# Kernel tuning notes

Measured on AMD Instinct MI355X. Metric: run time of the kernel, lower is better.

The kernel has to match this reference:

```python
import jax, jax.numpy as jnp
import numpy as np

B, IMGS, PH, PW = 4, 4, 16, 16      # 4 groups, 4 images/group, 16x16 patches per image
P, C = 16, 3
N = IMGS * PH * PW                   # 1024 packed tokens per group
PATCH_DIM = C * P * P                # 768
DIM, HEADS, DHEAD, DEPTH = 768, 12, 64, 4
INNER = HEADS * DHEAD
MLP = 3072
POSMAX = 32                          # image_size // patch_size
NCLS = 1000
SCALE = DHEAD ** 0.5


def _ln(x, g):
    # torch LayerNorm with learned gamma, beta frozen at 0
    mu = jnp.mean(x, -1, keepdims=True)
    var = jnp.var(x, -1, keepdims=True)
    return (x - mu) * jax.lax.rsqrt(var + 1e-5) * g


def _qk_rmsnorm(t, g):
    # F.normalize(t, dim=-1) * sqrt(dhead) * gamma[h, 1, d]; t: (b,h,n,d), g: (h,d)
    nrm = jnp.sqrt(jnp.sum(t * t, -1, keepdims=True))
    return t / jnp.maximum(nrm, 1e-12) * SCALE * g[None, :, None, :]


def _attention(x, context, ln_g, Wq, Wkv, qg, kg, Wo, attn_mask):
    xn = _ln(x, ln_g)
    kv_in = xn if context is None else context  # context is NOT normed (matches torch)
    q = xn @ Wq
    k, v = jnp.split(kv_in @ Wkv, 2, axis=-1)
    split = lambda t: t.reshape(t.shape[0], t.shape[1], HEADS, DHEAD).transpose(0, 2, 1, 3)
    q, k, v = split(q), split(k), split(v)
    q = _qk_rmsnorm(q, qg)
    k = _qk_rmsnorm(k, kg)
    dots = jnp.einsum('bhid,bhjd->bhij', q, k)  # no 1/sqrt(d): scale lives in RMSNorm
    dots = jnp.where(attn_mask, dots, -jnp.finfo(dots.dtype).max)
    attn = jax.nn.softmax(dots, axis=-1)
    out = jnp.einsum('bhij,bhjd->bhid', attn, v)
    out = out.transpose(0, 2, 1, 3).reshape(x.shape[0], -1, INNER)
    return out @ Wo


def _forward(patches, emb_ln_g, W_emb, b_emb, emb_ln2_g, pos_h, pos_w,
             ln_attn_g, Wq, Wkv, qn_g, kn_g, Wo,
             ln_ff_g, W1, b1, W2, b2, final_ln_g,
             pool_q, pool_ln_g, pWq, pWkv, p_qn_g, p_kn_g, pWo,
             head_ln_g, W_head,
             patch_positions, image_ids, lengths):
    valid = jnp.arange(N)[None, :] < lengths[:, None]              # (B,N) True = real token
    same_img = image_ids[:, :, None] == image_ids[:, None, :]      # (B,i,j) block-diagonal
    attn_mask = (same_img & valid[:, None, :])[:, None]            # (B,1,i,j)

    x = _ln(patches, emb_ln_g) @ W_emb + b_emb
    x = _ln(x, emb_ln2_g)
    x = x + pos_h[patch_positions[..., 0]] + pos_w[patch_positions[..., 1]]

    for l in range(DEPTH):
        x = _attention(x, None, ln_attn_g[l], Wq[l], Wkv[l], qn_g[l], kn_g[l], Wo[l], attn_mask) + x
        h = jax.nn.gelu(_ln(x, ln_ff_g[l]) @ W1[l] + b1[l], approximate=False)
        x = h @ W2[l] + b2[l] + x
    x = _ln(x, final_ln_g)

    # attention pooling: one learned query per packed image
    queries = jnp.broadcast_to(pool_q, (x.shape[0], IMGS, DIM))
    pool_mask = ((jnp.arange(IMGS)[None, :, None] == image_ids[:, None, :]) & valid[:, None, :])[:, None]
    pooled = _attention(queries, x, pool_ln_g, pWq, pWkv, p_qn_g, p_kn_g, pWo, pool_mask) + queries
    return _ln(pooled, head_ln_g) @ W_head  # (B, IMGS, NCLS), mlp_head has no bias


def setup_inputs():
    key = jax.random.key(0)
    ks = jax.random.split(key, 20)
    rn = lambda k, shape, s=0.02: (jax.random.normal(k, shape) * s).astype(jnp.float32)

    patches = jax.random.normal(ks[0], (B, N, PATCH_DIM), dtype=jnp.float32)
    hh, ww = jnp.meshgrid(jnp.arange(PH), jnp.arange(PW), indexing='ij')
    pos = jnp.stack([hh.reshape(-1), ww.reshape(-1)], axis=-1)        # (256,2)
    patch_positions = jnp.broadcast_to(jnp.tile(pos, (IMGS, 1))[None], (B, N, 2)).astype(jnp.int32)
    image_ids = jnp.broadcast_to(jnp.repeat(jnp.arange(IMGS), PH * PW)[None], (B, N)).astype(jnp.int32)
    lengths = jnp.full((B,), N, dtype=jnp.int32)

    return dict(
        patches=patches, patch_positions=patch_positions, image_ids=image_ids, lengths=lengths,
        emb_ln_g=jnp.ones(PATCH_DIM, jnp.float32), W_emb=rn(ks[1], (PATCH_DIM, DIM)),
        b_emb=jnp.zeros(DIM, jnp.float32), emb_ln2_g=jnp.ones(DIM, jnp.float32),
        pos_h=rn(ks[2], (POSMAX, DIM), 1.0), pos_w=rn(ks[3], (POSMAX, DIM), 1.0),
        ln_attn_g=jnp.ones((DEPTH, DIM), jnp.float32),
        Wq=rn(ks[4], (DEPTH, DIM, INNER)), Wkv=rn(ks[5], (DEPTH, DIM, 2 * INNER)),
        qn_g=jnp.ones((DEPTH, HEADS, DHEAD), jnp.float32), kn_g=jnp.ones((DEPTH, HEADS, DHEAD), jnp.float32),
        Wo=rn(ks[6], (DEPTH, INNER, DIM)),
        ln_ff_g=jnp.ones((DEPTH, DIM), jnp.float32),
        W1=rn(ks[7], (DEPTH, DIM, MLP)), b1=jnp.zeros((DEPTH, MLP), jnp.float32),
        W2=rn(ks[8], (DEPTH, MLP, DIM)), b2=jnp.zeros((DEPTH, DIM), jnp.float32),
        final_ln_g=jnp.ones(DIM, jnp.float32),
        pool_q=rn(ks[9], (DIM,), 1.0), pool_ln_g=jnp.ones(DIM, jnp.float32),
        pWq=rn(ks[10], (DIM, INNER)), pWkv=rn(ks[11], (DIM, 2 * INNER)),
        p_qn_g=jnp.ones((HEADS, DHEAD), jnp.float32), p_kn_g=jnp.ones((HEADS, DHEAD), jnp.float32),
        pWo=rn(ks[12], (INNER, DIM)),
        head_ln_g=jnp.ones(DIM, jnp.float32), W_head=rn(ks[13], (DIM, NCLS)),
    )


def reference(patches, patch_positions, image_ids, lengths,
              emb_ln_g, W_emb, b_emb, emb_ln2_g, pos_h, pos_w,
              ln_attn_g, Wq, Wkv, qn_g, kn_g, Wo,
              ln_ff_g, W1, b1, W2, b2, final_ln_g,
              pool_q, pool_ln_g, pWq, pWkv, p_qn_g, p_kn_g, pWo,
              head_ln_g, W_head):
    return _forward(patches, emb_ln_g, W_emb, b_emb, emb_ln2_g, pos_h, pos_w,
                    ln_attn_g, Wq, Wkv, qn_g, kn_g, Wo,
                    ln_ff_g, W1, b1, W2, b2, final_ln_g,
                    pool_q, pool_ln_g, pWq, pWkv, p_qn_g, p_kn_g, pWo,
                    head_ln_g, W_head, patch_positions, image_ids, lengths)
```

## Files before the change

kernel.cpp:

```cpp
#include <hip/hip_runtime.h>
#include <hip/hip_bf16.h>
#include <math.h>

using bf16 = __hip_bfloat16;
typedef short s16x8 __attribute__((ext_vector_type(8)));
typedef short s16x4 __attribute__((ext_vector_type(4)));
typedef float f32x4 __attribute__((ext_vector_type(4)));

#define DEVI __device__ __forceinline__

static constexpr int NB    = 4;
static constexpr int NTOK  = 1024;
static constexpr int DIM   = 768;
static constexpr int NH    = 12;
static constexpr int MLPD  = 3072;
static constexpr int NLAYER= 4;
static constexpr int NIMG  = 4;
static constexpr int NCLS  = 1000;
static constexpr int MR    = NB * NTOK;
static constexpr size_t SLAB = (size_t)MR * 768;

DEVI float b2f(bf16 v){ return __bfloat162float(v); }
DEVI bf16  f2b(float v){ return __float2bfloat16(v); }
DEVI float bu2f(unsigned short u){ union{unsigned u32; float f;} w; w.u32 = ((unsigned)u)<<16; return w.f; }
DEVI unsigned short f2bu(float f){ bf16 b = f2b(f); return *(unsigned short*)&b; }

DEVI void async16(const void* g, void* l) {
  __builtin_amdgcn_global_load_lds((const __attribute__((address_space(1))) void*)g,
                                   (__attribute__((address_space(3))) void*)l, 16, 0, 0);
}

DEVI f32x4 mfma16(s16x8 a, s16x8 b, f32x4 c) {
  return __builtin_amdgcn_mfma_f32_16x16x32_bf16(a, b, c, 0, 0, 0);
}

template<int N> DEVI void waitcnt_vm() {
  if constexpr (N == 0)      asm volatile("s_waitcnt vmcnt(0)" ::: "memory");
  else if constexpr (N == 3) asm volatile("s_waitcnt vmcnt(3)" ::: "memory");
  else if constexpr (N == 4) asm volatile("s_waitcnt vmcnt(4)" ::: "memory");
  else if constexpr (N == 6) asm volatile("s_waitcnt vmcnt(6)" ::: "memory");
}

DEVI float block_sum(float v, float* scratch, int tid) {
  #pragma unroll
  for (int o = 32; o >= 1; o >>= 1) v += __shfl_xor(v, o);
  __syncthreads();
  if ((tid & 63) == 0) scratch[tid >> 6] = v;
  __syncthreads();
  return scratch[0] + scratch[1] + scratch[2] + scratch[3];
}

DEVI float block_max(float v, float* scratch, int tid) {
  #pragma unroll
  for (int o = 32; o >= 1; o >>= 1) v = fmaxf(v, __shfl_xor(v, o));
  __syncthreads();
  if ((tid & 63) == 0) scratch[tid >> 6] = v;
  __syncthreads();
  return fmaxf(fmaxf(scratch[0], scratch[1]), fmaxf(scratch[2], scratch[3]));
}

struct TEntry { const float* src; bf16* dst; int R, C, tiles, tC; };
struct TDesc  { TEntry e[22]; };

__global__ __launch_bounds__(256) void transpose_kernel(TDesc D, int nent) {
  int bid = blockIdx.x, ei = 0;
  while (ei < nent - 1 && bid >= D.e[ei].tiles) { bid -= D.e[ei].tiles; ++ei; }
  const TEntry E = D.e[ei];
  const int tr = bid / E.tC, tc = bid % E.tC;
  __shared__ unsigned short t[64][68];
  const int tid = threadIdx.x;
  {
    const int r = tid >> 4, c = (tid & 15) * 4;
    float4 v[4];
    #pragma unroll
    for (int p = 0; p < 4; ++p)
      v[p] = *(const float4*)(E.src + (size_t)(tr*64 + p*16 + r)*E.C + tc*64 + c);
    #pragma unroll
    for (int p = 0; p < 4; ++p) {
      unsigned short* dst = &t[p*16 + r][c];
      dst[0] = f2bu(v[p].x); dst[1] = f2bu(v[p].y); dst[2] = f2bu(v[p].z); dst[3] = f2bu(v[p].w);
    }
  }
  __syncthreads();
  #pragma unroll
  for (int p = 0; p < 2; ++p) {
    const int n = p*32 + (tid >> 3);
    const int r0 = (tid & 7) * 8;
    s16x8 o;
    #pragma unroll
    for (int i = 0; i < 8; ++i) o[i] = (short)t[r0 + i][n];
    *(s16x8*)((short*)E.dst + (size_t)(tc*64 + n)*E.R + tr*64 + r0) = o;
  }
}

__global__ __launch_bounds__(256) void ln768_kernel(const float* __restrict__ in,
    const float* __restrict__ g, bf16* __restrict__ out)
{
  __shared__ float scratch[4];
  const int row = blockIdx.x, tid = threadIdx.x;
  const float* p = in + (size_t)row*768;
  const float v0 = p[tid], v1 = p[tid+256], v2 = p[tid+512];
  const float s  = block_sum(v0+v1+v2, scratch, tid);
  const float ss = block_sum(v0*v0+v1*v1+v2*v2, scratch, tid);
  const float mu = s * (1.0f/768.0f);
  const float var = ss * (1.0f/768.0f) - mu*mu;
  const float rstd = rsqrtf(var + 1e-5f);
  bf16* o = out + (size_t)row*768;
  o[tid]     = f2b((v0-mu)*rstd*g[tid]);
  o[tid+256] = f2b((v1-mu)*rstd*g[tid+256]);
  o[tid+512] = f2b((v2-mu)*rstd*g[tid+512]);
}

template<int HAS_BIAS>
__global__ __launch_bounds__(256) void res2_ln_kernel(float* __restrict__ x,
    const float* __restrict__ P, const float* __restrict__ bias,
    const float* __restrict__ g, bf16* __restrict__ xn)
{
  __shared__ float scratch[4];
  const int row = blockIdx.x, tid = threadIdx.x;
  const size_t base = (size_t)row*768;
  const float* p0 = P + base;
  const float* p1 = P + SLAB + base;
  float* xr = x + base;
  float v[3];
  #pragma unroll
  for (int i = 0; i < 3; ++i) {
    const int c = tid + i*256;
    float t = xr[c] + p0[c] + p1[c];
    if constexpr (HAS_BIAS) t += bias[c];
    v[i] = t;
    xr[c] = t;
  }
  const float s  = block_sum(v[0]+v[1]+v[2], scratch, tid);
  const float ss = block_sum(v[0]*v[0]+v[1]*v[1]+v[2]*v[2], scratch, tid);
  const float mu = s * (1.0f/768.0f);
  const float rstd = rsqrtf(ss*(1.0f/768.0f) - mu*mu + 1e-5f);
  bf16* o = xn + base;
  #pragma unroll
  for (int i = 0; i < 3; ++i) {
    const int c = tid + i*256;
    o[c] = f2b((v[i]-mu)*rstd*g[c]);
  }
}

__global__ __launch_bounds__(256) void ln_pos2_kernel(const float* __restrict__ P,
    const float* __restrict__ bias, const float* __restrict__ g,
    const float* __restrict__ pos_h, const float* __restrict__ pos_w,
    const int* __restrict__ ppos, float* __restrict__ out,
    const float* __restrict__ g2, bf16* __restrict__ xn)
{
  __shared__ float scratch[4];
  const int row = blockIdx.x, tid = threadIdx.x;
  const size_t base = (size_t)row*768;
  const float* p0 = P + base;
  const float* p1 = P + SLAB + base;
  float v[3];
  #pragma unroll
  for (int i = 0; i < 3; ++i) {
    const int c = tid + i*256;
    v[i] = p0[c] + p1[c] + bias[c];
  }
  const float s  = block_sum(v[0]+v[1]+v[2], scratch, tid);
  const float ss = block_sum(v[0]*v[0]+v[1]*v[1]+v[2]*v[2], scratch, tid);
  const float mu = s * (1.0f/768.0f);
  const float rstd = rsqrtf(ss*(1.0f/768.0f) - mu*mu + 1e-5f);
  const int p0i = ppos[row*2], p1i = ppos[row*2+1];
  const float* ph = pos_h + (size_t)p0i*768;
  const float* pw = pos_w + (size_t)p1i*768;
  float* o = out + base;
  float xv[3];
  #pragma unroll
  for (int i = 0; i < 3; ++i) {
    const int c = tid + i*256;
    xv[i] = (v[i]-mu)*rstd*g[c] + ph[c] + pw[c];
    o[c] = xv[i];
  }
  const float s2  = block_sum(xv[0]+xv[1]+xv[2], scratch, tid);
  const float ss2 = block_sum(xv[0]*xv[0]+xv[1]*xv[1]+xv[2]*xv[2], scratch, tid);
  const float mu2 = s2 * (1.0f/768.0f);
  const float rstd2 = rsqrtf(ss2*(1.0f/768.0f) - mu2*mu2 + 1e-5f);
  bf16* on = xn + base;
  #pragma unroll
  for (int i = 0; i < 3; ++i) {
    const int c = tid + i*256;
    on[c] = f2b((xv[i]-mu2)*rstd2*g2[c]);
  }
}

template<int DO_BIAS, int DO_GELU, int OUT_BF16, int DO_RES, int NTILE, int SPLITK, int RMSQKV>
__global__ __launch_bounds__(256)
void gemm_mfma(const bf16* __restrict__ A, const bf16* __restrict__ BT,
               const float* __restrict__ bias, float* __restrict__ Cf,
               bf16* __restrict__ Cb,
               const float* __restrict__ qg, const float* __restrict__ kg,
               bf16* __restrict__ Qp, bf16* __restrict__ Kp, bf16* __restrict__ Vp,
               int M, int Nn, int K)
{
  constexpr int NF  = NTILE / 32;
  constexpr int PD  = 3;
  constexpr int LPI = 2 + NTILE/64;
  constexpr int VW  = (PD - 2) * LPI;
  __shared__ bf16 As[PD][64*64];
  __shared__ bf16 Bs[PD][(NTILE/2)*64];
  const int tid = threadIdx.x;
  const int wid = tid >> 6, lane = tid & 63;
  const int quad = lane >> 4, l15 = lane & 15;
  const int wy = wid >> 1, wx = wid & 1;

  const int gx  = gridDim.x;
  const int nwg = gx * gridDim.y;
  const int bid = blockIdx.y * gx + blockIdx.x;
  const int qq  = nwg >> 3, rm = nwg & 7;
  const int xcd = bid & 7,  li = bid >> 3;
  const int swz = (xcd < rm ? xcd * (qq + 1) : rm * (qq + 1) + (xcd - rm) * qq) + li;
  const int m0 = (swz / gx) * 128, n0 = (swz % gx) * NTILE;

  const int kz    = (SPLITK > 1) ? blockIdx.z : 0;
  const int kloc  = K / SPLITK;
  const int kbase = kz * kloc;

  const int rl = lane >> 3;
  const int cs = lane & 7;

  f32x4 acc[4][NF];
  #pragma unroll
  for (int i = 0; i < 4; ++i)
    #pragma unroll
    for (int j = 0; j < NF; ++j) acc[i][j] = (f32x4){0.f,0.f,0.f,0.f};

  auto stage = [&](int buf, int k0) {
    #pragma unroll
    for (int c = 0; c < 2; ++c) {
      const int rbase = wid*8 + c*32;
      const int r_abs = rbase + rl;
      const int ceff  = cs ^ (r_abs & 7);
      const int mg    = 2*r_abs + (ceff >> 2);
      const int jb    = (ceff & 3) * 16;
      async16((const char*)A + ((size_t)(m0 + mg)*K + k0)*2 + jb, (char*)As[buf] + rbase*128);
    }
    #pragma unroll
    for (int c = 0; c < NTILE/64; ++c) {
      const int rbase = wid*8 + c*32;
      const int r_abs = rbase + rl;
      const int ceff  = cs ^ (r_abs & 7);
      const int ng    = 2*r_abs + (ceff >> 2);
      const int jb    = (ceff & 3) * 16;
      async16((const char*)BT + ((size_t)(n0 + ng)*K + k0)*2 + jb, (char*)Bs[buf] + rbase*128);
    }
  };

  auto compute = [&](int cb) {
    s16x8 af[4], bfr[NF];
    #pragma unroll
    for (int mt = 0; mt < 4; ++mt) {
      const int m = wy*64 + mt*16 + l15;
      const int r = m >> 1;
      const int cq = (((m & 1) << 2) | quad) ^ (r & 7);
      af[mt] = *(const s16x8*)((const char*)As[cb] + r*128 + cq*16);
    }
    #pragma unroll
    for (int nt = 0; nt < NF; ++nt) {
      const int n = wx*(NTILE/2) + nt*16 + l15;
      const int r = n >> 1;
      const int cq = (((n & 1) << 2) | quad) ^ (r & 7);
      bfr[nt] = *(const s16x8*)((const char*)Bs[cb] + r*128 + cq*16);
    }
    #pragma unroll
    for (int mt = 0; mt < 4; ++mt)
      #pragma unroll
      for (int nt = 0; nt < NF; ++nt)
        acc[mt][nt] = mfma16(af[mt], bfr[nt], acc[mt][nt]);
  };

  const int nk = kloc >> 5;
  #pragma unroll
  for (int t = 0; t < PD - 1; ++t) stage(t, kbase + (t << 5));

  int cbuf = 0, sbuf = PD - 1;
  const int mainN = nk - (PD - 1);
  for (int kt = 0; kt < mainN; ++kt) {
    __builtin_amdgcn_sched_barrier(0);
    waitcnt_vm<VW>();
    __builtin_amdgcn_s_barrier();
    __builtin_amdgcn_sched_barrier(0);
    stage(sbuf, kbase + ((kt + PD - 1) << 5));
    compute(cbuf);
    cbuf = (cbuf + 1 == PD) ? 0 : cbuf + 1;
    sbuf = (sbuf + 1 == PD) ? 0 : sbuf + 1;
  }
  for (int kt = mainN; kt < nk; ++kt) {
    __builtin_amdgcn_sched_barrier(0);
    waitcnt_vm<0>();
    __builtin_amdgcn_s_barrier();
    __builtin_amdgcn_sched_barrier(0);
    compute(cbuf);
    cbuf = (cbuf + 1 == PD) ? 0 : cbuf + 1;
  }

  if constexpr (RMSQKV) {
    __shared__ float red[128][2];
    const int hg = n0 >> 6;
    const int region = hg / NH;
    const int h  = hg - region*NH;
    const int b  = m0 >> 10;
    const int bh = b*NH + h;
    const int tokb = m0 & (NTOK-1);
    if (region < 2) {
      float sl[4][4];
      #pragma unroll
      for (int mt = 0; mt < 4; ++mt)
        #pragma unroll
        for (int rr = 0; rr < 4; ++rr) {
          float ssq = 0.f;
          #pragma unroll
          for (int nt = 0; nt < NF; ++nt) ssq += acc[mt][nt][rr]*acc[mt][nt][rr];
          #pragma unroll
          for (int o = 1; o <= 8; o <<= 1) ssq += __shfl_xor(ssq, o);
          sl[mt][rr] = ssq;
        }
      if (l15 == 0) {
        #pragma unroll
        for (int mt = 0; mt < 4; ++mt)
          #pragma unroll
          for (int rr = 0; rr < 4; ++rr)
            red[wy*64 + mt*16 + quad*4 + rr][wx] = sl[mt][rr];
      }
      __syncthreads();
      const float* gp = (region == 0) ? (qg + n0) : (kg + (n0 - 768));
      bf16* outb = (region == 0) ? Qp : Kp;
      #pragma unroll
      for (int mt = 0; mt < 4; ++mt)
        #pragma unroll
        for (int rr = 0; rr < 4; ++rr) {
          const int rlc = wy*64 + mt*16 + quad*4 + rr;
          const float rn = 8.0f / fmaxf(sqrtf(red[rlc][0] + red[rlc][1]), 1e-12f);
          const int tok = tokb + rlc;
          #pragma unroll
          for (int nt = 0; nt < NF; ++nt) {
            const int d = wx*32 + nt*16 + l15;
            outb[((size_t)bh*NTOK + tok)*64 + d] = f2b(acc[mt][nt][rr]*rn*gp[d]);
          }
        }
    } else {
      #pragma unroll
      for (int mt = 0; mt < 4; ++mt)
        #pragma unroll
        for (int nt = 0; nt < NF; ++nt) {
          const int d = wx*32 + nt*16 + l15;
          const int tok = tokb + wy*64 + mt*16 + quad*4;
          s16x4 pk;
          #pragma unroll
          for (int rr = 0; rr < 4; ++rr) pk[rr] = (short)f2bu(acc[mt][nt][rr]);
          *(s16x4*)((short*)Vp + ((size_t)bh*64 + d)*NTOK + tok) = pk;
        }
    }
  } else {
    float* Cslab = (SPLITK > 1) ? (Cf + (size_t)kz * SLAB) : Cf;
    #pragma unroll
    for (int nt = 0; nt < NF; ++nt) {
      const int col = n0 + wx*(NTILE/2) + nt*16 + l15;
      float bv = 0.f;
      if constexpr (DO_BIAS) bv = bias[col];
      #pragma unroll
      for (int mt = 0; mt < 4; ++mt) {
        #pragma unroll
        for (int r = 0; r < 4; ++r) {
          const int row = m0 + wy*64 + mt*16 + quad*4 + r;
          float v = acc[mt][nt][r];
          if constexpr (DO_BIAS) v += bv;
          if constexpr (DO_GELU) v = 0.5f*v*(1.0f + erff(v*0.70710678118654752f));
          const size_t idx = (size_t)row*Nn + col;
          if constexpr (OUT_BF16) Cb[idx] = f2b(v);
          else if constexpr (DO_RES) Cslab[idx] += v;
          else Cslab[idx] = v;
        }
      }
    }
  }
}

template<int IN_BF16, int DO_BIAS>
__global__ __launch_bounds__(256) void smallm_gemm(const void* __restrict__ Xv,
    const float* __restrict__ W, const float* __restrict__ bias,
    float* __restrict__ out, int Nn)
{
  __shared__ float Xs[16*768];
  __shared__ float red[4][16][64];
  const int tid = threadIdx.x;
  if constexpr (IN_BF16) {
    const bf16* X = (const bf16*)Xv;
    for (int i = tid; i < 16*768; i += 256) Xs[i] = b2f(X[i]);
  } else {
    const float* X = (const float*)Xv;
    for (int i = tid; i < 16*768; i += 256) Xs[i] = X[i];
  }
  __syncthreads();
  const int cl = tid & 63, kg = tid >> 6;
  const int c = blockIdx.x*64 + cl;
  float acc[16];
  #pragma unroll
  for (int r = 0; r < 16; ++r) acc[r] = 0.f;
  if (c < Nn) {
    const int k0 = kg*192;
    #pragma unroll 4
    for (int k = k0; k < k0 + 192; ++k) {
      const float w = W[(size_t)k*Nn + c];
      #pragma unroll
      for (int r = 0; r < 16; ++r) acc[r] += Xs[r*768 + k] * w;
    }
  }
  #pragma unroll
  for (int r = 0; r < 16; ++r) red[kg][r][cl] = acc[r];
  __syncthreads();
  if (kg == 0 && c < Nn) {
    #pragma unroll
    for (int r = 0; r < 16; ++r) {
      float v = red[0][r][cl] + red[1][r][cl] + red[2][r][cl] + red[3][r][cl];
      if constexpr (DO_BIAS) v += bias[c];
      out[(size_t)r*Nn + c] = v;
    }
  }
}

__global__ __launch_bounds__(256) void attn_mfma(const bf16* __restrict__ Qb,
    const bf16* __restrict__ Kb, const bf16* __restrict__ VTb, bf16* __restrict__ Ob,
    const int* __restrict__ ids, const int* __restrict__ lens)
{
  __shared__ bf16 Ps[4][16*72];
  __shared__ int  ids_s[NTOK];
  const int qt = blockIdx.x, h = blockIdx.y, b = blockIdx.z;
  const int tid = threadIdx.x;
  const int wid = tid >> 6, lane = tid & 63;
  const int quad = lane >> 4, l15 = lane & 15;
  const int bh = b*NH + h;
  const int q0 = qt*64;
  const int len = lens[b];

  #pragma unroll
  for (int i = 0; i < 4; ++i) ids_s[i*256 + tid] = ids[b*NTOK + i*256 + tid];
  __syncthreads();

  const bf16* qrow = Qb + ((size_t)bh*NTOK + q0 + wid*16 + l15)*64;
  const s16x8 aq0 = *(const s16x8*)(qrow + quad*8);
  const s16x8 aq1 = *(const s16x8*)(qrow + 32 + quad*8);

  int idq[4];
  #pragma unroll
  for (int rr = 0; rr < 4; ++rr) idq[rr] = ids_s[q0 + wid*16 + quad*4 + rr];

  unsigned qm = 0;
  #pragma unroll
  for (int rr = 0; rr < 4; ++rr) qm |= 1u << (idq[rr] & 31);
  #pragma unroll
  for (int o = 32; o >= 1; o >>= 1) qm |= (unsigned)__shfl_xor((int)qm, o);

  f32x4 oacc[4];
  #pragma unroll
  for (int nt = 0; nt < 4; ++nt) oacc[nt] = (f32x4){0.f,0.f,0.f,0.f};
  float mrow[4] = {-3.0e38f,-3.0e38f,-3.0e38f,-3.0e38f};
  float lrow[4] = {0.f,0.f,0.f,0.f};

  const bf16* Kgb = Kb  + (size_t)bh*NTOK*64;
  const bf16* Vgb = VTb + (size_t)bh*64*NTOK;
  bf16* pw = Ps[wid];

  for (int kt = 0; kt < 16; ++kt) {
    const int k0 = kt*64;
    const int idk_l = ids_s[k0 + lane];
    const bool ok = ((k0 + lane) < len) && (((qm >> (idk_l & 31)) & 1u) != 0u);
    if (__ballot(ok) == 0ULL) continue;

    f32x4 sA[4];
    #pragma unroll
    for (int jt = 0; jt < 4; ++jt) {
      const bf16* krow = Kgb + (size_t)(k0 + jt*16 + l15)*64;
      const s16x8 bk0 = *(const s16x8*)(krow + quad*8);
      const s16x8 bk1 = *(const s16x8*)(krow + 32 + quad*8);
      f32x4 s = (f32x4){0.f,0.f,0.f,0.f};
      s = mfma16(aq0, bk0, s);
      s = mfma16(aq1, bk1, s);
      sA[jt] = s;
    }
    #pragma unroll
    for (int jt = 0; jt < 4; ++jt) {
      const int j = k0 + jt*16 + l15;
      const int idk = ids_s[j];
      const bool kvld = j < len;
      #pragma unroll
      for (int rr = 0; rr < 4; ++rr)
        sA[jt][rr] = (kvld && idk == idq[rr]) ? sA[jt][rr] : -3.0e38f;
    }
    float alpha[4], mnew[4];
    #pragma unroll
    for (int rr = 0; rr < 4; ++rr) {
      float mx = fmaxf(fmaxf(sA[0][rr], sA[1][rr]), fmaxf(sA[2][rr], sA[3][rr]));
      mx = fmaxf(mx, __shfl_xor(mx, 1));
      mx = fmaxf(mx, __shfl_xor(mx, 2));
      mx = fmaxf(mx, __shfl_xor(mx, 4));
      mx = fmaxf(mx, __shfl_xor(mx, 8));
      const float mn = fmaxf(mrow[rr], mx);
      mnew[rr] = mn;
      alpha[rr] = expf(mrow[rr] - mn);
      mrow[rr] = mn;
    }
    #pragma unroll
    for (int rr = 0; rr < 4; ++rr) {
      float rs = 0.f;
      #pragma unroll
      for (int jt = 0; jt < 4; ++jt) {
        const float pv = (sA[jt][rr] > -1.0e38f) ? expf(sA[jt][rr] - mnew[rr]) : 0.0f;
        sA[jt][rr] = pv;
        rs += pv;
      }
      rs += __shfl_xor(rs, 1);
      rs += __shfl_xor(rs, 2);
      rs += __shfl_xor(rs, 4);
      rs += __shfl_xor(rs, 8);
      lrow[rr] = lrow[rr]*alpha[rr] + rs;
      #pragma unroll
      for (int nt = 0; nt < 4; ++nt) oacc[nt][rr] *= alpha[rr];
    }
    #pragma unroll
    for (int jt = 0; jt < 4; ++jt)
      #pragma unroll
      for (int rr = 0; rr < 4; ++rr)
        pw[(quad*4+rr)*72 + jt*16 + l15] = f2b(sA[jt][rr]);
    #pragma unroll
    for (int ss = 0; ss < 2; ++ss) {
      const s16x8 ap = *(const s16x8*)(pw + l15*72 + ss*32 + quad*8);
      #pragma unroll
      for (int nt = 0; nt < 4; ++nt) {
        const s16x8 bv = *(const s16x8*)(Vgb + (size_t)(nt*16 + l15)*NTOK + k0 + ss*32 + quad*8);
        oacc[nt] = mfma16(ap, bv, oacc[nt]);
      }
    }
  }

  #pragma unroll
  for (int rr = 0; rr < 4; ++rr) {
    const float inv = lrow[rr] > 0.f ? 1.0f/lrow[rr] : 0.0f;
    const int n = q0 + wid*16 + quad*4 + rr;
    bf16* orow = Ob + ((size_t)b*NTOK + n)*768 + h*64;
    #pragma unroll
    for (int nt = 0; nt < 4; ++nt)
      orow[nt*16 + l15] = f2b(oacc[nt][rr]*inv);
  }
}

__global__ __launch_bounds__(256) void pool_q_kernel(const float* __restrict__ pool_q,
    const float* __restrict__ pool_ln_g, const float* __restrict__ pWq,
    const float* __restrict__ p_qn_g, float* __restrict__ qp)
{
  __shared__ float xn[768];
  __shared__ float scratch[4];
  __shared__ float qraw[64];
  const int h = blockIdx.x, tid = threadIdx.x;
  float v0 = pool_q[tid], v1 = pool_q[tid+256], v2 = pool_q[tid+512];
  const float s  = block_sum(v0+v1+v2, scratch, tid);
  const float ss = block_sum(v0*v0+v1*v1+v2*v2, scratch, tid);
  const float mu = s*(1.0f/768.0f);
  const float rstd = rsqrtf(ss*(1.0f/768.0f) - mu*mu + 1e-5f);
  xn[tid]     = (v0-mu)*rstd*pool_ln_g[tid];
  xn[tid+256] = (v1-mu)*rstd*pool_ln_g[tid+256];
  xn[tid+512] = (v2-mu)*rstd*pool_ln_g[tid+512];
  __syncthreads();
  const int d = tid >> 2, pp = tid & 3;
  const int col = h*64 + d;
  float acc = 0.f;
  for (int k = pp*192; k < (pp+1)*192; ++k) acc += xn[k]*pWq[(size_t)k*768 + col];
  acc += __shfl_xor(acc, 1); acc += __shfl_xor(acc, 2);
  if (pp == 0) qraw[d] = acc;
  __syncthreads();
  if (tid < 64) {
    const float q = qraw[tid];
    float sq = q*q;
    #pragma unroll
    for (int o = 32; o >= 1; o >>= 1) sq += __shfl_xor(sq, o);
    const float rn = 8.0f / fmaxf(sqrtf(sq), 1e-12f);
    qp[h*64 + tid] = q * rn * p_qn_g[h*64 + tid];
  }
}

__global__ __launch_bounds__(256) void pool_attn_kernel(const bf16* __restrict__ kvp,
    const float* __restrict__ qp, const float* __restrict__ kg,
    const int* __restrict__ ids, const int* __restrict__ lens, float* __restrict__ pooled)
{
  __shared__ float sp[1024];
  __shared__ float qg_s[64];
  __shared__ float scratch[4];
  __shared__ float outred[4][64];
  const int h = blockIdx.x, img = blockIdx.y, b = blockIdx.z;
  const int tid = threadIdx.x;
  const int len = lens[b];
  if (tid < 64) qg_s[tid] = qp[h*64 + tid] * kg[h*64 + tid];
  __syncthreads();

  float smax = -3.0e38f;
  for (int j = tid; j < 1024; j += 256) {
    float sv = -3.0e38f;
    if (j < len && ids[b*NTOK + j] == img) {
      const bf16* kr = kvp + (size_t)(b*NTOK + j)*1536 + h*64;
      float ssq = 0.f, dq = 0.f;
      #pragma unroll
      for (int dd = 0; dd < 64; dd += 8) {
        s16x8 k8 = *(const s16x8*)(kr + dd);
        #pragma unroll
        for (int i = 0; i < 8; ++i) {
          const float kv = bu2f((unsigned short)k8[i]);
          ssq += kv*kv;
          dq  += qg_s[dd+i]*kv;
        }
      }
      const float rn = 8.0f / fmaxf(sqrtf(ssq), 1e-12f);
      sv = dq * rn;
    }
    sp[j] = sv;
    smax = fmaxf(smax, sv);
  }
  const float M = block_max(smax, scratch, tid);
  float lsum = 0.f;
  for (int j = tid; j < 1024; j += 256) {
    const float p = (sp[j] > -1.0e38f) ? expf(sp[j] - M) : 0.0f;
    sp[j] = p;
    lsum += p;
  }
  const float L = block_sum(lsum, scratch, tid);
  const float invL = L > 0.f ? 1.0f / L : 0.0f;

  const int d = tid & 63, jg = tid >> 6;
  float acc = 0.f;
  for (int j = jg; j < 1024; j += 4) {
    const float p = sp[j];
    if (p > 0.f) acc += p * b2f(kvp[(size_t)(b*NTOK + j)*1536 + 768 + h*64 + d]);
  }
  outred[jg][d] = acc;
  __syncthreads();
  if (tid < 64) {
    const float o = (outred[0][tid] + outred[1][tid] + outred[2][tid] + outred[3][tid]) * invL;
    pooled[((size_t)b*NIMG + img)*768 + h*64 + tid] = o;
  }
}

extern "C" void kernel_launch(void* const* d_in, const int* in_sizes, int n_in,
                              void* d_out, int out_size, void* d_ws, size_t ws_size,
                              hipStream_t stream)
{
  const float* patches    = (const float*)d_in[0];
  const int*   ppos       = (const int*)d_in[1];
  const int*   image_ids  = (const int*)d_in[2];
  const int*   lengths    = (const int*)d_in[3];
  const float* emb_ln_g   = (const float*)d_in[4];
  const float* W_emb      = (const float*)d_in[5];
  const float* b_emb      = (const float*)d_in[6];
  const float* emb_ln2_g  = (const float*)d_in[7];
  const float* pos_h      = (const float*)d_in[8];
  const float* pos_w      = (const float*)d_in[9];
  const float* ln_attn_g  = (const float*)d_in[10];
  const float* Wq         = (const float*)d_in[11];
  const float* Wkv        = (const float*)d_in[12];
  const float* qn_g       = (const float*)d_in[13];
  const float* kn_g       = (const float*)d_in[14];
  const float* Wo         = (const float*)d_in[15];
  const float* ln_ff_g    = (const float*)d_in[16];
  const float* W1         = (const float*)d_in[17];
  const float* b1         = (const float*)d_in[18];
  const float* W2         = (const float*)d_in[19];
  const float* b2v        = (const float*)d_in[20];
  const float* final_ln_g = (const float*)d_in[21];
  const float* pool_q     = (const float*)d_in[22];
  const float* pool_ln_g  = (const float*)d_in[23];
  const float* pWq        = (const float*)d_in[24];
  const float* pWkv       = (const float*)d_in[25];
  const float* p_qn_g     = (const float*)d_in[26];
  const float* p_kn_g     = (const float*)d_in[27];
  const float* pWo        = (const float*)d_in[28];
  const float* head_ln_g  = (const float*)d_in[29];
  const float* W_head     = (const float*)d_in[30];

  char* ws = (char*)d_ws;
  size_t off = 0;
  auto alloc = [&](size_t sz){ size_t r = off; off += (sz + 255) & ~(size_t)255; return r; };

  const size_t o_WembT = alloc((size_t)768*768*2);
  size_t o_QKVT[4], o_WoT[4], o_W1T[4], o_W2T[4];
  for (int l = 0; l < NLAYER; ++l) {
    o_QKVT[l] = alloc((size_t)2304*768*2);
    o_WoT[l]  = alloc((size_t)768*768*2);
    o_W1T[l]  = alloc((size_t)3072*768*2);
    o_W2T[l]  = alloc((size_t)768*3072*2);
  }
  const size_t o_pWkvT = alloc((size_t)1536*768*2);
  const size_t o_x     = alloc((size_t)MR*768*4);
  const size_t o_xn    = alloc((size_t)MR*768*2);
  const size_t o_kv    = alloc((size_t)MR*3072*2);
  const size_t o_P     = alloc((size_t)2*SLAB*4);
  const size_t o_Qb    = alloc((size_t)MR*768*2);
  const size_t o_Kb    = alloc((size_t)MR*768*2);
  const size_t o_VT    = alloc((size_t)MR*768*2);
  const size_t o_Ob    = alloc((size_t)MR*768*2);
  const size_t o_qp    = alloc((size_t)768*4);
  const size_t o_pool  = alloc((size_t)16*768*4);
  const size_t o_poolf = alloc((size_t)16*768*4);
  const size_t o_hl    = alloc((size_t)16*768*2);
  if (off > ws_size) return;

  float* x    = (float*)(ws + o_x);
  bf16*  xn   = (bf16*)(ws + o_xn);
  bf16*  hb   = (bf16*)(ws + o_kv);
  bf16*  kvb  = (bf16*)(ws + o_kv);
  float* P    = (float*)(ws + o_P);
  bf16*  Qb   = (bf16*)(ws + o_Qb);
  bf16*  Kb   = (bf16*)(ws + o_Kb);
  bf16*  VTb  = (bf16*)(ws + o_VT);
  bf16*  Ob   = (bf16*)(ws + o_Ob);
  float* qp   = (float*)(ws + o_qp);
  float* pooled  = (float*)(ws + o_pool);
  float* pooledf = (float*)(ws + o_poolf);
  bf16*  hl   = (bf16*)(ws + o_hl);

  TDesc td; int ne = 0, total = 0;
  auto add = [&](const float* s, size_t dofs, int R, int C){
    td.e[ne].src = s;
    td.e[ne].dst = (bf16*)(ws + dofs);
    td.e[ne].R = R; td.e[ne].C = C;
    td.e[ne].tiles = (R/64)*(C/64); td.e[ne].tC = C/64;
    total += td.e[ne].tiles; ++ne;
  };
  add(W_emb, o_WembT, 768, 768);
  for (int l = 0; l < NLAYER; ++l) {
    add(Wq  + (size_t)l*768*768,  o_QKVT[l],                 768, 768);
    add(Wkv + (size_t)l*768*1536, o_QKVT[l] + (size_t)768*768*2, 768, 1536);
    add(Wo  + (size_t)l*768*768,  o_WoT[l],                  768, 768);
    add(W1  + (size_t)l*768*3072, o_W1T[l],                  768, 3072);
    add(W2  + (size_t)l*3072*768, o_W2T[l],                  3072, 768);
  }
  add(pWkv, o_pWkvT, 768, 1536);
  transpose_kernel<<<total, 256, 0, stream>>>(td, ne);

  ln768_kernel<<<MR, 256, 0, stream>>>(patches, emb_ln_g, xn);
  gemm_mfma<0,0,0,0,64,2,0><<<dim3(12,32,2), 256, 0, stream>>>(xn, (const bf16*)(ws+o_WembT), nullptr,
      P, nullptr, nullptr, nullptr, nullptr, nullptr, nullptr, MR, 768, 768);
  ln_pos2_kernel<<<MR, 256, 0, stream>>>(P, b_emb, emb_ln2_g, pos_h, pos_w, ppos, x, ln_attn_g, xn);

  for (int l = 0; l < NLAYER; ++l) {
    gemm_mfma<0,0,0,0,64,1,1><<<dim3(36,32), 256, 0, stream>>>(xn, (const bf16*)(ws+o_QKVT[l]), nullptr,
        nullptr, nullptr, qn_g + (size_t)l*768, kn_g + (size_t)l*768, Qb, Kb, VTb, MR, 2304, 768);
    attn_mfma<<<dim3(16,NH,NB), 256, 0, stream>>>(Qb, Kb, VTb, Ob, image_ids, lengths);
    gemm_mfma<0,0,0,0,64,2,0><<<dim3(12,32,2), 256, 0, stream>>>(Ob, (const bf16*)(ws+o_WoT[l]), nullptr,
        P, nullptr, nullptr, nullptr, nullptr, nullptr, nullptr, MR, 768, 768);
    res2_ln_kernel<0><<<MR, 256, 0, stream>>>(x, P, nullptr, ln_ff_g + (size_t)l*768, xn);
    gemm_mfma<1,1,1,0,128,1,0><<<dim3(24,32), 256, 0, stream>>>(xn, (const bf16*)(ws+o_W1T[l]), b1 + (size_t)l*3072,
        nullptr, hb, nullptr, nullptr, nullptr, nullptr, nullptr, MR, 3072, 768);
    gemm_mfma<0,0,0,0,64,2,0><<<dim3(12,32,2), 256, 0, stream>>>(hb, (const bf16*)(ws+o_W2T[l]), nullptr,
        P, nullptr, nullptr, nullptr, nullptr, nullptr, nullptr, MR, 768, 3072);
    const float* gnext = (l + 1 < NLAYER) ? (ln_attn_g + (size_t)(l+1)*768) : final_ln_g;
    res2_ln_kernel<1><<<MR, 256, 0, stream>>>(x, P, b2v + (size_t)l*768, gnext, xn);
  }

  gemm_mfma<0,0,1,0,64,1,0><<<dim3(24,32), 256, 0, stream>>>(xn, (const bf16*)(ws+o_pWkvT), nullptr,
      nullptr, kvb, nullptr, nullptr, nullptr, nullptr, nullptr, MR, 1536, 768);
  pool_q_kernel<<<NH, 256, 0, stream>>>(pool_q, pool_ln_g, pWq, p_qn_g, qp);
  pool_attn_kernel<<<dim3(NH,NIMG,NB), 256, 0, stream>>>(kvb, qp, p_kn_g, image_ids, lengths, pooled);
  smallm_gemm<0,1><<<12, 256, 0, stream>>>(pooled, pWo, pool_q, pooledf, 768);
  ln768_kernel<<<16, 256, 0, stream>>>(pooledf, head_ln_g, hl);
  smallm_gemm<1,0><<<16, 256, 0, stream>>>(hl, W_head, nullptr, (float*)d_out, NCLS);
}
```

Baseline: 1.089 ms.

## Replace split-K GEMMs with BM=64 tiles and fuse residual/bias into epilogue

Removes split-K from the 768-wide output GEMMs and uses 64-row M tiles instead. The Wo and W2 GEMMs now add their results, with bias, directly into the residual stream. This turns the res2_ln kernels into plain LayerNorm kernels and drops the second partial-sum slab, cutting global-memory traffic for the fp32 partials. The embedding GEMM gets its bias fused in, and the weight transpose kernel moves to 128x128 tiles. In exchange the narrow GEMMs do their full K reduction per block, which makes each block's loop longer.

```diff
diff --git a/kernel.cpp b/kernel.cpp
--- a/kernel.cpp
+++ b/kernel.cpp
@@ -36,6 +36,7 @@
 
 template<int N> DEVI void waitcnt_vm() {
   if constexpr (N == 0)      asm volatile("s_waitcnt vmcnt(0)" ::: "memory");
+  else if constexpr (N == 2) asm volatile("s_waitcnt vmcnt(2)" ::: "memory");
   else if constexpr (N == 3) asm volatile("s_waitcnt vmcnt(3)" ::: "memory");
   else if constexpr (N == 4) asm volatile("s_waitcnt vmcnt(4)" ::: "memory");
   else if constexpr (N == 6) asm volatile("s_waitcnt vmcnt(6)" ::: "memory");
@@ -67,29 +68,31 @@
   while (ei < nent - 1 && bid >= D.e[ei].tiles) { bid -= D.e[ei].tiles; ++ei; }
   const TEntry E = D.e[ei];
   const int tr = bid / E.tC, tc = bid % E.tC;
-  __shared__ unsigned short t[64][68];
+  __shared__ unsigned short t[128][132];
   const int tid = threadIdx.x;
   {
-    const int r = tid >> 4, c = (tid & 15) * 4;
-    float4 v[4];
-    #pragma unroll
-    for (int p = 0; p < 4; ++p)
-      v[p] = *(const float4*)(E.src + (size_t)(tr*64 + p*16 + r)*E.C + tc*64 + c);
-    #pragma unroll
-    for (int p = 0; p < 4; ++p) {
-      unsigned short* dst = &t[p*16 + r][c];
+    const int c = (tid & 31) * 4;
+    const int rb = tid >> 5;
+    float4 v[16];
+    #pragma unroll
+    for (int p = 0; p < 16; ++p)
+      v[p] = *(const float4*)(E.src + (size_t)(tr*128 + p*8 + rb)*E.C + tc*128 + c);
+    #pragma unroll
+    for (int p = 0; p < 16; ++p) {
+      unsigned short* dst = &t[p*8 + rb][c];
       dst[0] = f2bu(v[p].x); dst[1] = f2bu(v[p].y); dst[2] = f2bu(v[p].z); dst[3] = f2bu(v[p].w);
     }
   }
   __syncthreads();
-  #pragma unroll
-  for (int p = 0; p < 2; ++p) {
-    const int n = p*32 + (tid >> 3);
-    const int r0 = (tid & 7) * 8;
+  const int n  = tid >> 1;
+  const int kh = (tid & 1) * 64;
+  #pragma unroll
+  for (int p = 0; p < 8; ++p) {
+    const int r0 = kh + p*8;
     s16x8 o;
     #pragma unroll
     for (int i = 0; i < 8; ++i) o[i] = (short)t[r0 + i][n];
-    *(s16x8*)((short*)E.dst + (size_t)(tc*64 + n)*E.R + tr*64 + r0) = o;
+    *(s16x8*)((short*)E.dst + (size_t)(tc*128 + n)*E.R + tr*128 + r0) = o;
   }
 }
 
@@ -111,40 +114,8 @@
   o[tid+512] = f2b((v2-mu)*rstd*g[tid+512]);
 }
 
-template<int HAS_BIAS>
-__global__ __launch_bounds__(256) void res2_ln_kernel(float* __restrict__ x,
-    const float* __restrict__ P, const float* __restrict__ bias,
-    const float* __restrict__ g, bf16* __restrict__ xn)
-{
-  __shared__ float scratch[4];
-  const int row = blockIdx.x, tid = threadIdx.x;
-  const size_t base = (size_t)row*768;
-  const float* p0 = P + base;
-  const float* p1 = P + SLAB + base;
-  float* xr = x + base;
-  float v[3];
-  #pragma unroll
-  for (int i = 0; i < 3; ++i) {
-    const int c = tid + i*256;
-    float t = xr[c] + p0[c] + p1[c];
-    if constexpr (HAS_BIAS) t += bias[c];
-    v[i] = t;
-    xr[c] = t;
-  }
-  const float s  = block_sum(v[0]+v[1]+v[2], scratch, tid);
-  const float ss = block_sum(v[0]*v[0]+v[1]*v[1]+v[2]*v[2], scratch, tid);
-  const float mu = s * (1.0f/768.0f);
-  const float rstd = rsqrtf(ss*(1.0f/768.0f) - mu*mu + 1e-5f);
-  bf16* o = xn + base;
-  #pragma unroll
-  for (int i = 0; i < 3; ++i) {
-    const int c = tid + i*256;
-    o[c] = f2b((v[i]-mu)*rstd*g[c]);
-  }
-}
-
 __global__ __launch_bounds__(256) void ln_pos2_kernel(const float* __restrict__ P,
-    const float* __restrict__ bias, const float* __restrict__ g,
+    const float* __restrict__ g,
     const float* __restrict__ pos_h, const float* __restrict__ pos_w,
     const int* __restrict__ ppos, float* __restrict__ out,
     const float* __restrict__ g2, bf16* __restrict__ xn)
@@ -153,13 +124,9 @@
   const int row = blockIdx.x, tid = threadIdx.x;
   const size_t base = (size_t)row*768;
   const float* p0 = P + base;
-  const float* p1 = P + SLAB + base;
   float v[3];
   #pragma unroll
-  for (int i = 0; i < 3; ++i) {
-    const int c = tid + i*256;
-    v[i] = p0[c] + p1[c] + bias[c];
-  }
+  for (int i = 0; i < 3; ++i) v[i] = p0[tid + i*256];
   const float s  = block_sum(v[0]+v[1]+v[2], scratch, tid);
   const float ss = block_sum(v[0]*v[0]+v[1]*v[1]+v[2]*v[2], scratch, tid);
   const float mu = s * (1.0f/768.0f);
@@ -187,7 +154,7 @@
   }
 }
 
-template<int DO_BIAS, int DO_GELU, int OUT_BF16, int DO_RES, int NTILE, int SPLITK, int RMSQKV>
+template<int DO_BIAS, int DO_GELU, int OUT_BF16, int DO_RES, int BM, int NTILE, int RMSQKV>
 __global__ __launch_bounds__(256)
 void gemm_mfma(const bf16* __restrict__ A, const bf16* __restrict__ BT,
                const float* __restrict__ bias, float* __restrict__ Cf,
@@ -196,12 +163,13 @@
                bf16* __restrict__ Qp, bf16* __restrict__ Kp, bf16* __restrict__ Vp,
                int M, int Nn, int K)
 {
+  constexpr int MF  = BM / 32;
   constexpr int NF  = NTILE / 32;
   constexpr int PD  = 3;
-  constexpr int LPI = 2 + NTILE/64;
+  constexpr int LPI = BM/64 + NTILE/64;
   constexpr int VW  = (PD - 2) * LPI;
-  __shared__ bf16 As[PD][64*64];
-  __shared__ bf16 Bs[PD][(NTILE/2)*64];
+  __shared__ bf16 As[PD][BM*32];
+  __shared__ bf16 Bs[PD][NTILE*32];
   const int tid = threadIdx.x;
   const int wid = tid >> 6, lane = tid & 63;
   const int quad = lane >> 4, l15 = lane & 15;
@@ -213,24 +181,20 @@
   const int qq  = nwg >> 3, rm = nwg & 7;
   const int xcd = bid & 7,  li = bid >> 3;
   const int swz = (xcd < rm ? xcd * (qq + 1) : rm * (qq + 1) + (xcd - rm) * qq) + li;
-  const int m0 = (swz / gx) * 128, n0 = (swz % gx) * NTILE;
-
-  const int kz    = (SPLITK > 1) ? blockIdx.z : 0;
-  const int kloc  = K / SPLITK;
-  const int kbase = kz * kloc;
+  const int m0 = (swz / gx) * BM, n0 = (swz % gx) * NTILE;
 
   const int rl = lane >> 3;
   const int cs = lane & 7;
 
-  f32x4 acc[4][NF];
-  #pragma unroll
-  for (int i = 0; i < 4; ++i)
+  f32x4 acc[MF][NF];
+  #pragma unroll
+  for (int i = 0; i < MF; ++i)
     #pragma unroll
     for (int j = 0; j < NF; ++j) acc[i][j] = (f32x4){0.f,0.f,0.f,0.f};
 
   auto stage = [&](int buf, int k0) {
     #pragma unroll
-    for (int c = 0; c < 2; ++c) {
+    for (int c = 0; c < BM/64; ++c) {
       const int rbase = wid*8 + c*32;
       const int r_abs = rbase + rl;
       const int ceff  = cs ^ (r_abs & 7);
@@ -250,10 +214,10 @@
   };
 
   auto compute = [&](int cb) {
-    s16x8 af[4], bfr[NF];
-    #pragma unroll
-    for (int mt = 0; mt < 4; ++mt) {
-      const int m = wy*64 + mt*16 + l15;
+    s16x8 af[MF], bfr[NF];
+    #pragma unroll
+    for (int mt = 0; mt < MF; ++mt) {
+      const int m = wy*(BM/2) + mt*16 + l15;
       const int r = m >> 1;
       const int cq = (((m & 1) << 2) | quad) ^ (r & 7);
       af[mt] = *(const s16x8*)((const char*)As[cb] + r*128 + cq*16);
@@ -266,15 +230,15 @@
       bfr[nt] = *(const s16x8*)((const char*)Bs[cb] + r*128 + cq*16);
     }
     #pragma unroll
-    for (int mt = 0; mt < 4; ++mt)
+    for (int mt = 0; mt < MF; ++mt)
       #pragma unroll
       for (int nt = 0; nt < NF; ++nt)
         acc[mt][nt] = mfma16(af[mt], bfr[nt], acc[mt][nt]);
   };
 
-  const int nk = kloc >> 5;
-  #pragma unroll
-  for (int t = 0; t < PD - 1; ++t) stage(t, kbase + (t << 5));
+  const int nk = K >> 5;
+  #pragma unroll
+  for (int t = 0; t < PD - 1; ++t) stage(t, t << 5);
 
   int cbuf = 0, sbuf = PD - 1;
   const int mainN = nk - (PD - 1);
@@ -283,7 +247,7 @@
     waitcnt_vm<VW>();
     __builtin_amdgcn_s_barrier();
     __builtin_amdgcn_sched_barrier(0);
-    stage(sbuf, kbase + ((kt + PD - 1) << 5));
+    stage(sbuf, (kt + PD - 1) << 5);
     compute(cbuf);
     cbuf = (cbuf + 1 == PD) ? 0 : cbuf + 1;
     sbuf = (sbuf + 1 == PD) ? 0 : sbuf + 1;
@@ -306,9 +270,9 @@
     const int bh = b*NH + h;
     const int tokb = m0 & (NTOK-1);
     if (region < 2) {
-      float sl[4][4];
-      #pragma unroll
-      for (int mt = 0; mt < 4; ++mt)
+      float sl[MF][4];
+      #pragma unroll
+      for (int mt = 0; mt < MF; ++mt)
         #pragma unroll
         for (int rr = 0; rr < 4; ++rr) {
           float ssq = 0.f;
@@ -320,19 +284,19 @@
         }
       if (l15 == 0) {
         #pragma unroll
-        for (int mt = 0; mt < 4; ++mt)
+        for (int mt = 0; mt < MF; ++mt)
           #pragma unroll
           for (int rr = 0; rr < 4; ++rr)
-            red[wy*64 + mt*16 + quad*4 + rr][wx] = sl[mt][rr];
+            red[wy*(BM/2) + mt*16 + quad*4 + rr][wx] = sl[mt][rr];
       }
       __syncthreads();
       const float* gp = (region == 0) ? (qg + n0) : (kg + (n0 - 768));
       bf16* outb = (region == 0) ? Qp : Kp;
       #pragma unroll
-      for (int mt = 0; mt < 4; ++mt)
+      for (int mt = 0; mt < MF; ++mt)
         #pragma unroll
         for (int rr = 0; rr < 4; ++rr) {
-          const int rlc = wy*64 + mt*16 + quad*4 + rr;
+          const int rlc = wy*(BM/2) + mt*16 + quad*4 + rr;
           const float rn = 8.0f / fmaxf(sqrtf(red[rlc][0] + red[rlc][1]), 1e-12f);
           const int tok = tokb + rlc;
           #pragma unroll
@@ -343,11 +307,11 @@
         }
     } else {
       #pragma unroll
-      for (int mt = 0; mt < 4; ++mt)
+      for (int mt = 0; mt < MF; ++mt)
         #pragma unroll
         for (int nt = 0; nt < NF; ++nt) {
           const int d = wx*32 + nt*16 + l15;
-          const int tok = tokb + wy*64 + mt*16 + quad*4;
+          const int tok = tokb + wy*(BM/2) + mt*16 + quad*4;
           s16x4 pk;
           #pragma unroll
           for (int rr = 0; rr < 4; ++rr) pk[rr] = (short)f2bu(acc[mt][nt][rr]);
@@ -355,24 +319,23 @@
         }
     }
   } else {
-    float* Cslab = (SPLITK > 1) ? (Cf + (size_t)kz * SLAB) : Cf;
     #pragma unroll
     for (int nt = 0; nt < NF; ++nt) {
       const int col = n0 + wx*(NTILE/2) + nt*16 + l15;
       float bv = 0.f;
       if constexpr (DO_BIAS) bv = bias[col];
       #pragma unroll
-      for (int mt = 0; mt < 4; ++mt) {
+      for (int mt = 0; mt < MF; ++mt) {
         #pragma unroll
         for (int r = 0; r < 4; ++r) {
-          const int row = m0 + wy*64 + mt*16 + quad*4 + r;
+          const int row = m0 + wy*(BM/2) + mt*16 + quad*4 + r;
           float v = acc[mt][nt][r];
           if constexpr (DO_BIAS) v += bv;
           if constexpr (DO_GELU) v = 0.5f*v*(1.0f + erff(v*0.70710678118654752f));
           const size_t idx = (size_t)row*Nn + col;
           if constexpr (OUT_BF16) Cb[idx] = f2b(v);
-          else if constexpr (DO_RES) Cslab[idx] += v;
-          else Cslab[idx] = v;
+          else if constexpr (DO_RES) Cf[idx] += v;
+          else Cf[idx] = v;
         }
       }
     }
@@ -693,7 +656,7 @@
   const size_t o_x     = alloc((size_t)MR*768*4);
   const size_t o_xn    = alloc((size_t)MR*768*2);
   const size_t o_kv    = alloc((size_t)MR*3072*2);
-  const size_t o_P     = alloc((size_t)2*SLAB*4);
+  const size_t o_P     = alloc(SLAB*4);
   const size_t o_Qb    = alloc((size_t)MR*768*2);
   const size_t o_Kb    = alloc((size_t)MR*768*2);
   const size_t o_VT    = alloc((size_t)MR*768*2);
@@ -723,7 +686,7 @@
     td.e[ne].src = s;
     td.e[ne].dst = (bf16*)(ws + dofs);
     td.e[ne].R = R; td.e[ne].C = C;
-    td.e[ne].tiles = (R/64)*(C/64); td.e[ne].tC = C/64;
+    td.e[ne].tiles = (R/128)*(C/128); td.e[ne].tC = C/128;
     total += td.e[ne].tiles; ++ne;
   };
   add(W_emb, o_WembT, 768, 768);
@@ -738,26 +701,26 @@
   transpose_kernel<<<total, 256, 0, stream>>>(td, ne);
 
   ln768_kernel<<<MR, 256, 0, stream>>>(patches, emb_ln_g, xn);
-  gemm_mfma<0,0,0,0,64,2,0><<<dim3(12,32,2), 256, 0, stream>>>(xn, (const bf16*)(ws+o_WembT), nullptr,
+  gemm_mfma<1,0,0,0,64,64,0><<<dim3(12,64), 256, 0, stream>>>(xn, (const bf16*)(ws+o_WembT), b_emb,
       P, nullptr, nullptr, nullptr, nullptr, nullptr, nullptr, MR, 768, 768);
-  ln_pos2_kernel<<<MR, 256, 0, stream>>>(P, b_emb, emb_ln2_g, pos_h, pos_w, ppos, x, ln_attn_g, xn);
+  ln_pos2_kernel<<<MR, 256, 0, stream>>>(P, emb_ln2_g, pos_h, pos_w, ppos, x, ln_attn_g, xn);
 
   for (int l = 0; l < NLAYER; ++l) {
-    gemm_mfma<0,0,0,0,64,1,1><<<dim3(36,32), 256, 0, stream>>>(xn, (const bf16*)(ws+o_QKVT[l]), nullptr,
+    gemm_mfma<0,0,0,0,128,64,1><<<dim3(36,32), 256, 0, stream>>>(xn, (const bf16*)(ws+o_QKVT[l]), nullptr,
         nullptr, nullptr, qn_g + (size_t)l*768, kn_g + (size_t)l*768, Qb, Kb, VTb, MR, 2304, 768);
     attn_mfma<<<dim3(16,NH,NB), 256, 0, stream>>>(Qb, Kb, VTb, Ob, image_ids, lengths);
-    gemm_mfma<0,0,0,0,64,2,0><<<dim3(12,32,2), 256, 0, stream>>>(Ob, (const bf16*)(ws+o_WoT[l]), nullptr,
-        P, nullptr, nullptr, nullptr, nullptr, nullptr, nullptr, MR, 768, 768);
-    res2_ln_kernel<0><<<MR, 256, 0, stream>>>(x, P, nullptr, ln_ff_g + (size_t)l*768, xn);
-    gemm_mfma<1,1,1,0,128,1,0><<<dim3(24,32), 256, 0, stream>>>(xn, (const bf16*)(ws+o_W1T[l]), b1 + (size_t)l*3072,
+    gemm_mfma<0,0,0,1,64,64,0><<<dim3(12,64), 256, 0, stream>>>(Ob, (const bf16*)(ws+o_WoT[l]), nullptr,
+        x, nullptr, nullptr, nullptr, nullptr, nullptr, nullptr, MR, 768, 768);
+    ln768_kernel<<<MR, 256, 0, stream>>>(x, ln_ff_g + (size_t)l*768, xn);
+    gemm_mfma<1,1,1,0,128,128,0><<<dim3(24,32), 256, 0, stream>>>(xn, (const bf16*)(ws+o_W1T[l]), b1 + (size_t)l*3072,
         nullptr, hb, nullptr, nullptr, nullptr, nullptr, nullptr, MR, 3072, 768);
-    gemm_mfma<0,0,0,0,64,2,0><<<dim3(12,32,2), 256, 0, stream>>>(hb, (const bf16*)(ws+o_W2T[l]), nullptr,
-        P, nullptr, nullptr, nullptr, nullptr, nullptr, nullptr, MR, 768, 3072);
+    gemm_mfma<1,0,0,1,64,64,0><<<dim3(12,64), 256, 0, stream>>>(hb, (const bf16*)(ws+o_W2T[l]), b2v + (size_t)l*768,
+        x, nullptr, nullptr, nullptr, nullptr, nullptr, nullptr, MR, 768, 3072);
     const float* gnext = (l + 1 < NLAYER) ? (ln_attn_g + (size_t)(l+1)*768) : final_ln_g;
-    res2_ln_kernel<1><<<MR, 256, 0, stream>>>(x, P, b2v + (size_t)l*768, gnext, xn);
-  }
-
-  gemm_mfma<0,0,1,0,64,1,0><<<dim3(24,32), 256, 0, stream>>>(xn, (const bf16*)(ws+o_pWkvT), nullptr,
+    ln768_kernel<<<MR, 256, 0, stream>>>(x, gnext, xn);
+  }
+
+  gemm_mfma<0,0,1,0,128,64,0><<<dim3(24,32), 256, 0, stream>>>(xn, (const bf16*)(ws+o_pWkvT), nullptr,
       nullptr, kvb, nullptr, nullptr, nullptr, nullptr, nullptr, MR, 1536, 768);
   pool_q_kernel<<<NH, 256, 0, stream>>>(pool_q, pool_ln_g, pWq, p_qn_g, qp);
   pool_attn_kernel<<<dim3(NH,NIMG,NB), 256, 0, stream>>>(kvb, qp, p_kn_g, image_ids, lengths, pooled);
```

Result: slower. 1.121 ms (+3.0%).
